# Optimization experiments

Measured on AMD Instinct MI355X. Metric: run time of the kernel, lower is better.

Reference implementation:

```python
import jax, jax.numpy as jnp
import numpy as np

N = 100000        # num nodes
E2 = 3200000      # num directed edges (symmetric)
D = 256           # node feature dim
C = 40            # num classes
NIDS = 1000       # labelled node ids
TOL = 0.01
MAXITER = 16
AVG_DEG = E2 // N // 2 * 2  # ~32


def setup_inputs() -> dict:
    key = jax.random.key(0)
    k1, k2, k3, k4, k5, k6 = jax.random.split(key, 6)
    E = E2 // 2
    row_h = jax.random.randint(k1, (E,), 0, N, dtype=jnp.int32)
    col_h = jax.random.randint(k2, (E,), 0, N, dtype=jnp.int32)
    # symmetrize so I - (1-eps)*A is SPD-like (CG assumption)
    row = jnp.concatenate([row_h, col_h])
    col = jnp.concatenate([col_h, row_h])
    vals = jax.random.uniform(k3, (E,), dtype=jnp.float32) * (0.9 / 32.0)
    data = jnp.concatenate([vals, vals])
    node_features = jax.random.normal(k4, (N, D), dtype=jnp.float32)
    ids = jax.random.randint(k5, (NIDS,), 0, N, dtype=jnp.int32)
    # hk.Linear with TruncatedNormal(stddev=1/sqrt(D)) init
    W = (jax.random.truncated_normal(k6, -2.0, 2.0, (D, C), dtype=jnp.float32)
         * (1.0 / np.sqrt(D))).astype(jnp.float32)
    b = jnp.zeros((C,), jnp.float32)
    e0 = jnp.zeros((), jnp.float32)  # hk.get_parameter('e0', (), init=zeros)
    return dict(node_features=node_features, W=W, b=b, e0=e0,
                data=data, row=row, col=col, ids=ids)


def reference(node_features, W, b, e0, data, row, col, ids):
    epsilon = jax.nn.sigmoid(e0)
    # head_transform=None; d_feat > num_classes -> Linear first, then smooth
    x = node_features @ W + b  # [N, C]

    def spmv(v):  # adj @ v for COO adjacency, v: [N, C]
        return jax.ops.segment_sum(data[:, None] * v[col], row, num_segments=N)

    def f(v):  # (I - (1-eps) A) v
        return v - (1.0 - epsilon) * spmv(v)

    # smooth(): x.shape[1] (=C) <= ids.size -> direct CG on dense x, then gather ids
    sol, _ = jax.scipy.sparse.linalg.cg(f, x, tol=TOL, maxiter=MAXITER)
    return sol[ids]  # [NIDS, C] logits
```

## Files before the change

### kernel.cpp

```cpp
#include <hip/hip_runtime.h>
#include <hip/hip_fp16.h>
#include <math.h>

#define NNODE  100000
#define NEDGE  3200000
#define DFEAT  256
#define NCLS   40
#define NC_TOT 4000000
#define NIDS   1000
#define TOLSQ  1.0e-4f
#define MAXIT  16

#define SB 2048
#define SLOT_TOT 1000000
#define SPB 489
#define XB 1024
#define VT 256
#define GR     128
#define GKC    32
#define GEMM_B 782

#define RB      128
#define NBUCK   782
#define BCAP    6144
#define SUBB    1024
#define NPB     800
#define EPB     4000

__device__ __forceinline__ float block_reduce_256(float v, float* red) {
  int tid = threadIdx.x;
  red[tid] = v;
  __syncthreads();
  #pragma unroll
  for (int off = 128; off > 0; off >>= 1) {
    if (tid < off) red[tid] += red[tid + off];
    __syncthreads();
  }
  float res = red[0];
  __syncthreads();
  return res;
}

__global__ void __launch_bounds__(256) k_pcount(const int* __restrict__ row,
                                                int* __restrict__ cntmat,
                                                int* __restrict__ total) {
  __shared__ int h[NBUCK];
  int tid = threadIdx.x, blk = blockIdx.x;
  for (int i = tid; i < NBUCK; i += 256) h[i] = 0;
  __syncthreads();
  int e0 = blk * EPB;
  for (int i = tid; i < EPB; i += 256) atomicAdd(&h[row[e0 + i] >> 7], 1);
  __syncthreads();
  for (int i = tid; i < NBUCK; i += 256) {
    int v = h[i];
    cntmat[blk * NBUCK + i] = v;
    if (v) atomicAdd(&total[i], v);
  }
}

__global__ void k_bscan2(const int* __restrict__ total, int* __restrict__ bptr) {
  __shared__ int s[1024];
  int tid = threadIdx.x;
  int v = (tid < NBUCK) ? total[tid] : 0;
  s[tid] = v;
  __syncthreads();
  for (int off = 1; off < 1024; off <<= 1) {
    int t = (tid >= off) ? s[tid - off] : 0;
    __syncthreads();
    s[tid] += t;
    __syncthreads();
  }
  if (tid < NBUCK) bptr[tid] = s[tid] - v;
  if (tid == 0) bptr[NBUCK] = NEDGE;
}

__global__ void __launch_bounds__(1024) k_colscan(int* __restrict__ cntmat,
                                                  const int* __restrict__ bptr) {
  __shared__ int s[1024];
  int b = blockIdx.x;
  int tid = threadIdx.x;
  int v = (tid < NPB) ? cntmat[tid * NBUCK + b] : 0;
  s[tid] = v;
  __syncthreads();
  for (int off = 1; off < 1024; off <<= 1) {
    int t = (tid >= off) ? s[tid - off] : 0;
    __syncthreads();
    s[tid] += t;
    __syncthreads();
  }
  if (tid < NPB) cntmat[tid * NBUCK + b] = bptr[b] + s[tid] - v;
}

__global__ void __launch_bounds__(256) k_ppart(const int* __restrict__ row,
    const int* __restrict__ col, const float* __restrict__ data,
    const int* __restrict__ offmat, uint2* __restrict__ bstage) {
  __shared__ int cnt[NBUCK];
  __shared__ int segs[NBUCK + 1];
  __shared__ int cur[NBUCK];
  __shared__ int goff[NBUCK];
  __shared__ int scp[256];
  __shared__ unsigned short bof[EPB];
  __shared__ uint2 pay[EPB];
  int tid = threadIdx.x, blk = blockIdx.x;
  int e0 = blk * EPB;

  for (int i = tid; i < NBUCK; i += 256) {
    cnt[i] = 0;
    goff[i] = offmat[blk * NBUCK + i];
  }
  __syncthreads();
  for (int i = tid; i < EPB; i += 256) atomicAdd(&cnt[row[e0 + i] >> 7], 1);
  __syncthreads();

  int t4 = tid * 4;
  int l0 = (t4 + 0 < NBUCK) ? cnt[t4 + 0] : 0;
  int l1 = (t4 + 1 < NBUCK) ? cnt[t4 + 1] : 0;
  int l2 = (t4 + 2 < NBUCK) ? cnt[t4 + 2] : 0;
  int l3 = (t4 + 3 < NBUCK) ? cnt[t4 + 3] : 0;
  int mysum = l0 + l1 + l2 + l3;
  scp[tid] = mysum;
  __syncthreads();
  for (int off = 1; off < 256; off <<= 1) {
    int t = (tid >= off) ? scp[tid - off] : 0;
    __syncthreads();
    scp[tid] += t;
    __syncthreads();
  }
  int base = scp[tid] - mysum;
  if (t4 + 0 <= NBUCK) segs[t4 + 0] = base;  base += l0;
  if (t4 + 1 <= NBUCK) segs[t4 + 1] = base;  base += l1;
  if (t4 + 2 <= NBUCK) segs[t4 + 2] = base;  base += l2;
  if (t4 + 3 <= NBUCK) segs[t4 + 3] = base;
  for (int i = tid; i < NBUCK; i += 256) cur[i] = 0;
  __syncthreads();

  for (int b = tid; b < NBUCK; b += 256) {
    int s1 = segs[b + 1];
    for (int i = segs[b]; i < s1; ++i) bof[i] = (unsigned short)b;
  }
  for (int i = tid; i < EPB; i += 256) {
    int rr = row[e0 + i];
    int b = rr >> 7;
    int rk = atomicAdd(&cur[b], 1);
    pay[segs[b] + rk] = make_uint2(((unsigned)(rr & (RB - 1)) << 17) | (unsigned)col[e0 + i],
                                   __float_as_uint(data[e0 + i]));
  }
  __syncthreads();
  for (int i = tid; i < EPB; i += 256) {
    int b = bof[i];
    bstage[goff[b] + (i - segs[b])] = pay[i];
  }
}

__global__ void __launch_bounds__(256) k_bbuild(const int* __restrict__ bptr,
    const uint2* __restrict__ bstage, int* __restrict__ rowptr,
    int2* __restrict__ csr) {
  __shared__ uint2 ebuf[BCAP];
  __shared__ int deg[SUBB];
  __shared__ int segs[SUBB];
  __shared__ int scp[256];
  int b = blockIdx.x;
  int s0 = bptr[b], s1 = bptr[b + 1];
  int n = s1 - s0;
  if (n > BCAP) n = BCAP;
  int tid = threadIdx.x;
  for (int i = tid; i < SUBB; i += 256) deg[i] = 0;
  __syncthreads();
  for (int i = tid; i < n; i += 256) {
    uint2 e = bstage[s0 + i];
    ebuf[i] = e;
    int key = (int)(e.x >> 17) * 8 + (int)((e.x & 0x1FFFF) >> 14);
    atomicAdd(&deg[key], 1);
  }
  __syncthreads();
  int t4 = tid * 4;
  int l0 = deg[t4 + 0], l1 = deg[t4 + 1], l2 = deg[t4 + 2], l3 = deg[t4 + 3];
  int mysum = l0 + l1 + l2 + l3;
  scp[tid] = mysum;
  __syncthreads();
  for (int off = 1; off < 256; off <<= 1) {
    int t = (tid >= off) ? scp[tid - off] : 0;
    __syncthreads();
    scp[tid] += t;
    __syncthreads();
  }
  int base = scp[tid] - mysum;
  segs[t4 + 0] = base;  base += l0;
  segs[t4 + 1] = base;  base += l1;
  segs[t4 + 2] = base;  base += l2;
  segs[t4 + 3] = base;
  __syncthreads();
  for (int i = tid; i < SUBB; i += 256) deg[i] = 0;
  if (tid < RB) {
    int grow = b * RB + tid;
    if (grow < NNODE) rowptr[grow] = s0 + segs[tid * 8];
  }
  if (b == 0 && tid == 0) rowptr[NNODE] = NEDGE;
  __syncthreads();
  for (int i = tid; i < n; i += 256) {
    uint2 e = ebuf[i];
    int col = (int)(e.x & 0x1FFFF);
    int key = (int)(e.x >> 17) * 8 + (col >> 14);
    int pos = atomicAdd(&deg[key], 1);
    csr[s0 + segs[key] + pos] = make_int2(col, (int)e.y);
  }
}

__global__ void __launch_bounds__(256) k_gemm(const float* __restrict__ feat,
    const float* __restrict__ W, const float* __restrict__ bias,
    float* __restrict__ r, float* __restrict__ p, __half* __restrict__ ph,
    float* __restrict__ part) {
  __shared__ float ftile[2][GR][GKC + 1];
  __shared__ float wtile[2][GKC * NCLS];
  __shared__ float red[256];
  int tid = threadIdx.x;
  int r0 = blockIdx.x * GR;
  int rl0 = (tid >> 2) * 2;
  int cbase = (tid & 3) * 10;
  float acc0[10], acc1[10];
  #pragma unroll
  for (int j = 0; j < 10; ++j) {
    float bv = bias[cbase + j];
    acc0[j] = bv;
    acc1[j] = bv;
  }

  float4 sf[4];
  float sw[5];
  int srr[4], skq[4];
  #pragma unroll
  for (int it = 0; it < 4; ++it) {
    int i = tid + it * 256;
    srr[it] = i >> 3;
    skq[it] = i & 7;
  }

  #pragma unroll
  for (int it = 0; it < 4; ++it) {
    int grow = r0 + srr[it];
    sf[it] = make_float4(0.f, 0.f, 0.f, 0.f);
    if (grow < NNODE)
      sf[it] = *(const float4*)(feat + (size_t)grow * DFEAT + skq[it] * 4);
  }
  #pragma unroll
  for (int it = 0; it < 5; ++it) sw[it] = W[tid + it * 256];
  #pragma unroll
  for (int it = 0; it < 4; ++it) {
    ftile[0][srr[it]][skq[it] * 4 + 0] = sf[it].x;
    ftile[0][srr[it]][skq[it] * 4 + 1] = sf[it].y;
    ftile[0][srr[it]][skq[it] * 4 + 2] = sf[it].z;
    ftile[0][srr[it]][skq[it] * 4 + 3] = sf[it].w;
  }
  #pragma unroll
  for (int it = 0; it < 5; ++it) wtile[0][tid + it * 256] = sw[it];
  __syncthreads();

  for (int t = 0; t < DFEAT / GKC; ++t) {
    if (t + 1 < DFEAT / GKC) {
      int k0n = (t + 1) * GKC;
      #pragma unroll
      for (int it = 0; it < 4; ++it) {
        int grow = r0 + srr[it];
        sf[it] = make_float4(0.f, 0.f, 0.f, 0.f);
        if (grow < NNODE)
          sf[it] = *(const float4*)(feat + (size_t)grow * DFEAT + k0n + skq[it] * 4);
      }
      #pragma unroll
      for (int it = 0; it < 5; ++it) sw[it] = W[k0n * NCLS + tid + it * 256];
    }
    int buf = t & 1;
    #pragma unroll 4
    for (int kk = 0; kk < GKC; ++kk) {
      float f0 = ftile[buf][rl0][kk];
      float f1 = ftile[buf][rl0 + 1][kk];
      const float* wr = &wtile[buf][kk * NCLS + cbase];
      #pragma unroll
      for (int j = 0; j < 10; ++j) {
        float w = wr[j];
        acc0[j] = fmaf(f0, w, acc0[j]);
        acc1[j] = fmaf(f1, w, acc1[j]);
      }
    }
    if (t + 1 < DFEAT / GKC) {
      int nb = (t + 1) & 1;
      #pragma unroll
      for (int it = 0; it < 4; ++it) {
        ftile[nb][srr[it]][skq[it] * 4 + 0] = sf[it].x;
        ftile[nb][srr[it]][skq[it] * 4 + 1] = sf[it].y;
        ftile[nb][srr[it]][skq[it] * 4 + 2] = sf[it].z;
        ftile[nb][srr[it]][skq[it] * 4 + 3] = sf[it].w;
      }
      #pragma unroll
      for (int it = 0; it < 5; ++it) wtile[nb][tid + it * 256] = sw[it];
      __syncthreads();
    }
  }

  float local = 0.f;
  int g0 = r0 + rl0, g1 = g0 + 1;
  if (g0 < NNODE) {
    size_t b0 = (size_t)g0 * NCLS + cbase;
    #pragma unroll
    for (int j = 0; j < 10; ++j) {
      float a = acc0[j];
      r[b0 + j] = a; p[b0 + j] = a; ph[b0 + j] = __float2half(a);
      local = fmaf(a, a, local);
    }
  }
  if (g1 < NNODE) {
    size_t b1 = (size_t)g1 * NCLS + cbase;
    #pragma unroll
    for (int j = 0; j < 10; ++j) {
      float a = acc1[j];
      r[b1 + j] = a; p[b1 + j] = a; ph[b1 + j] = __float2half(a);
      local = fmaf(a, a, local);
    }
  }
  float tot = block_reduce_256(local, red);
  if (tid == 0) part[blockIdx.x] = tot;
}

__global__ void k_init_scal(const float* __restrict__ part, const float* __restrict__ e0,
                            float* __restrict__ scal) {
  __shared__ float red[256];
  float local = 0.f;
  for (int i = threadIdx.x; i < GEMM_B; i += 256) local += part[i];
  float bs = block_reduce_256(local, red);
  if (threadIdx.x == 0) {
    float eps = 1.f / (1.f + expf(-e0[0]));
    scal[0] = 1.f - eps;
    scal[1] = TOLSQ * bs;
    scal[2] = bs;
  }
}

__global__ void __launch_bounds__(VT) k_spmv(const float* __restrict__ scal, int k,
    const int* __restrict__ rowptr, const int2* __restrict__ csr,
    const __half* __restrict__ ph, const float* __restrict__ p,
    float* __restrict__ Ap, float* __restrict__ part) {
  float gamma = scal[2 + k], atol2 = scal[1];
  if (!(gamma > atol2)) return;
  float omega = scal[0];
  int b = blockIdx.x;
  int chunk = (b & 7) * (SB / 8) + (b >> 3);
  int sbase = chunk * SPB;
  float local = 0.f;
  #pragma unroll
  for (int it = 0; it < 2; ++it) {
    int li = threadIdx.x + it * VT;
    int s = sbase + li;
    if (li < SPB && s < SLOT_TOT) {
      int rr = s / 10;
      int cq4 = (s - rr * 10) * 4;
      int s0 = rowptr[rr], s1 = rowptr[rr + 1];
      float a0 = 0.f, a1 = 0.f, a2 = 0.f, a3 = 0.f;
      #pragma unroll 4
      for (int j = s0; j < s1; ++j) {
        int2 pr = csr[j];
        float w = __int_as_float(pr.y);
        uint2 g = *(const uint2*)(ph + (size_t)pr.x * NCLS + cq4);
        __half2 h01 = *(__half2*)&g.x;
        __half2 h23 = *(__half2*)&g.y;
        float2 f01 = __half22float2(h01);
        float2 f23 = __half22float2(h23);
        a0 = fmaf(w, f01.x, a0);
        a1 = fmaf(w, f01.y, a1);
        a2 = fmaf(w, f23.x, a2);
        a3 = fmaf(w, f23.y, a3);
      }
      size_t e = (size_t)rr * NCLS + cq4;
      float4 pe = *(const float4*)(p + e);
      float4 v;
      v.x = fmaf(-omega, a0, pe.x);
      v.y = fmaf(-omega, a1, pe.y);
      v.z = fmaf(-omega, a2, pe.z);
      v.w = fmaf(-omega, a3, pe.w);
      *(float4*)(Ap + e) = v;
      local = fmaf(pe.x, v.x, local);
      local = fmaf(pe.y, v.y, local);
      local = fmaf(pe.z, v.z, local);
      local = fmaf(pe.w, v.w, local);
    }
  }
  __shared__ float red[256];
  float tot = block_reduce_256(local, red);
  if (threadIdx.x == 0) part[blockIdx.x] = tot;
}

__global__ void __launch_bounds__(VT) k_xr(const float* __restrict__ scal, int k,
    const float* __restrict__ part_in,
    const float* __restrict__ p, const float* __restrict__ Ap,
    float* __restrict__ r, const int* __restrict__ ids,
    float* __restrict__ out, float* __restrict__ part_out) {
  float gamma = scal[2 + k], atol2 = scal[1];
  if (!(gamma > atol2)) return;
  __shared__ float red[256];
  float lp = 0.f;
  for (int i = threadIdx.x; i < SB; i += VT) lp += part_in[i];
  float pap = block_reduce_256(lp, red);
  float alpha = gamma / pap;
  int idx = blockIdx.x * VT + threadIdx.x;
  if (idx < NIDS * NCLS) {
    int i = idx / NCLS, c = idx - (idx / NCLS) * NCLS;
    out[idx] += alpha * p[(size_t)ids[i] * NCLS + c];
  }
  const float4* a4 = (const float4*)Ap;
  float4* r4 = (float4*)r;
  float local = 0.f;
  int stride = gridDim.x * blockDim.x;
  for (int e = blockIdx.x * blockDim.x + threadIdx.x; e < NC_TOT / 4; e += stride) {
    float4 ae = a4[e], re = r4[e];
    re.x = fmaf(-alpha, ae.x, re.x); re.y = fmaf(-alpha, ae.y, re.y);
    re.z = fmaf(-alpha, ae.z, re.z); re.w = fmaf(-alpha, ae.w, re.w);
    r4[e] = re;
    local = fmaf(re.x, re.x, local); local = fmaf(re.y, re.y, local);
    local = fmaf(re.z, re.z, local); local = fmaf(re.w, re.w, local);
  }
  float tot = block_reduce_256(local, red);
  if (threadIdx.x == 0) part_out[blockIdx.x] = tot;
}

__global__ void __launch_bounds__(VT) k_pupd(float* __restrict__ scal, int k,
    const float* __restrict__ part_in,
    const float* __restrict__ r, float* __restrict__ p, __half* __restrict__ ph) {
  float gamma = scal[2 + k], atol2 = scal[1];
  if (!(gamma > atol2)) {
    if (blockIdx.x == 0 && threadIdx.x == 0) scal[2 + k + 1] = gamma;
    return;
  }
  __shared__ float red[256];
  float lp = 0.f;
  for (int i = threadIdx.x; i < XB; i += VT) lp += part_in[i];
  float gnew = block_reduce_256(lp, red);
  float beta = gnew / gamma;
  const float4* r4 = (const float4*)r;
  float4* p4 = (float4*)p;
  int stride = gridDim.x * blockDim.x;
  for (int e = blockIdx.x * blockDim.x + threadIdx.x; e < NC_TOT / 4; e += stride) {
    float4 pe = p4[e], re = r4[e];
    pe.x = fmaf(beta, pe.x, re.x); pe.y = fmaf(beta, pe.y, re.y);
    pe.z = fmaf(beta, pe.z, re.z); pe.w = fmaf(beta, pe.w, re.w);
    p4[e] = pe;
    int e4 = e * 4;
    ph[e4 + 0] = __float2half(pe.x);
    ph[e4 + 1] = __float2half(pe.y);
    ph[e4 + 2] = __float2half(pe.z);
    ph[e4 + 3] = __float2half(pe.w);
  }
  if (blockIdx.x == 0 && threadIdx.x == 0) scal[2 + k + 1] = gnew;
}

extern "C" void kernel_launch(void* const* d_in, const int* in_sizes, int n_in,
                              void* d_out, int out_size, void* d_ws, size_t ws_size,
                              hipStream_t stream) {
  const float* feat = (const float*)d_in[0];
  const float* W    = (const float*)d_in[1];
  const float* bias = (const float*)d_in[2];
  const float* e0   = (const float*)d_in[3];
  const float* data = (const float*)d_in[4];
  const int*   row  = (const int*)d_in[5];
  const int*   col  = (const int*)d_in[6];
  const int*   ids  = (const int*)d_in[7];
  float* out = (float*)d_out;

  size_t off = 0;
  char* base = (char*)d_ws;
  auto take = [&](size_t nbytes) -> void* {
    void* ptr = base + off;
    off += (nbytes + 255) & ~(size_t)255;
    return ptr;
  };
  float* rv  = (float*)take((size_t)NC_TOT * 4);
  float* pv  = (float*)take((size_t)NC_TOT * 4);
  float* ap  = (float*)take((size_t)NC_TOT * 4);
  __half* ph = (__half*)take((size_t)NC_TOT * 2);
  int2*  csr = (int2*)take((size_t)NEDGE * 8);
  int* rowptr    = (int*)take((size_t)(NNODE + 1) * 4);
  int* cntmat    = (int*)take((size_t)NPB * NBUCK * 4);
  int* total     = (int*)take((size_t)(NBUCK + 2) * 4);
  int* bptr      = (int*)take((size_t)(NBUCK + 2) * 4);
  float* part_a  = (float*)take(SB * 4);
  float* part_b  = (float*)take(XB * 4);
  float* scal    = (float*)take(64 * 4);

  uint2* bstage = (uint2*)rv;

  hipMemsetAsync(total, 0, (size_t)(NBUCK + 2) * 4, stream);
  hipMemsetAsync(out, 0, (size_t)NIDS * NCLS * 4, stream);
  k_pcount<<<NPB, 256, 0, stream>>>(row, cntmat, total);
  k_bscan2<<<1, 1024, 0, stream>>>(total, bptr);
  k_colscan<<<NBUCK, 1024, 0, stream>>>(cntmat, bptr);
  k_ppart<<<NPB, 256, 0, stream>>>(row, col, data, cntmat, bstage);
  k_bbuild<<<NBUCK, 256, 0, stream>>>(bptr, bstage, rowptr, csr);

  k_gemm<<<GEMM_B, 256, 0, stream>>>(feat, W, bias, rv, pv, ph, part_a);
  k_init_scal<<<1, 256, 0, stream>>>(part_a, e0, scal);

  for (int k = 0; k < MAXIT; ++k) {
    k_spmv<<<SB, VT, 0, stream>>>(scal, k, rowptr, csr, ph, pv, ap, part_a);
    k_xr  <<<XB, VT, 0, stream>>>(scal, k, part_a, pv, ap, rv, ids, out, part_b);
    k_pupd<<<XB, VT, 0, stream>>>(scal, k, part_b, rv, pv, ph);
  }
}
```

Before: 421.7 us.

## Split half-precision search vector into two 20-class column groups for SpMV gathers

Stores the fp16 copy of p as two separate planes of 20 classes per node instead of one 40-class row. The SpMV handles one plane at a time per block, so the gather footprint per pass is half the size and can stay in cache better. The GEMM and p-update kernels write the new layout, and the p-update now packs its fp16 stores into a single 8-byte write. The cost is that the CSR index and weight stream is read twice per SpMV, once per plane.

```diff
diff --git a/kernel.cpp b/kernel.cpp
--- a/kernel.cpp
+++ b/kernel.cpp
@@ -11,9 +11,10 @@
 #define TOLSQ  1.0e-4f
 #define MAXIT  16
 
-#define SB 2048
-#define SLOT_TOT 1000000
-#define SPB 489
+#define SB 1536
+#define SLOT_G 500000
+#define SPB2 326
+#define GRP_H 2000000
 #define XB 1024
 #define VT 256
 #define GR     128
@@ -217,6 +218,8 @@
   int r0 = blockIdx.x * GR;
   int rl0 = (tid >> 2) * 2;
   int cbase = (tid & 3) * 10;
+  int gg = (cbase >= 20) ? 1 : 0;
+  int cqb = cbase - gg * 20;
   float acc0[10], acc1[10];
   #pragma unroll
   for (int j = 0; j < 10; ++j) {
@@ -300,19 +303,21 @@
   int g0 = r0 + rl0, g1 = g0 + 1;
   if (g0 < NNODE) {
     size_t b0 = (size_t)g0 * NCLS + cbase;
+    size_t h0 = (size_t)gg * GRP_H + (size_t)g0 * 20 + cqb;
     #pragma unroll
     for (int j = 0; j < 10; ++j) {
       float a = acc0[j];
-      r[b0 + j] = a; p[b0 + j] = a; ph[b0 + j] = __float2half(a);
+      r[b0 + j] = a; p[b0 + j] = a; ph[h0 + j] = __float2half(a);
       local = fmaf(a, a, local);
     }
   }
   if (g1 < NNODE) {
     size_t b1 = (size_t)g1 * NCLS + cbase;
+    size_t h1 = (size_t)gg * GRP_H + (size_t)g1 * 20 + cqb;
     #pragma unroll
     for (int j = 0; j < 10; ++j) {
       float a = acc1[j];
-      r[b1 + j] = a; p[b1 + j] = a; ph[b1 + j] = __float2half(a);
+      r[b1 + j] = a; p[b1 + j] = a; ph[h1 + j] = __float2half(a);
       local = fmaf(a, a, local);
     }
   }
@@ -343,43 +348,47 @@
   float omega = scal[0];
   int b = blockIdx.x;
   int chunk = (b & 7) * (SB / 8) + (b >> 3);
-  int sbase = chunk * SPB;
+  int sbase = chunk * SPB2;
   float local = 0.f;
   #pragma unroll
-  for (int it = 0; it < 2; ++it) {
-    int li = threadIdx.x + it * VT;
-    int s = sbase + li;
-    if (li < SPB && s < SLOT_TOT) {
-      int rr = s / 10;
-      int cq4 = (s - rr * 10) * 4;
-      int s0 = rowptr[rr], s1 = rowptr[rr + 1];
-      float a0 = 0.f, a1 = 0.f, a2 = 0.f, a3 = 0.f;
-      #pragma unroll 4
-      for (int j = s0; j < s1; ++j) {
-        int2 pr = csr[j];
-        float w = __int_as_float(pr.y);
-        uint2 g = *(const uint2*)(ph + (size_t)pr.x * NCLS + cq4);
-        __half2 h01 = *(__half2*)&g.x;
-        __half2 h23 = *(__half2*)&g.y;
-        float2 f01 = __half22float2(h01);
-        float2 f23 = __half22float2(h23);
-        a0 = fmaf(w, f01.x, a0);
-        a1 = fmaf(w, f01.y, a1);
-        a2 = fmaf(w, f23.x, a2);
-        a3 = fmaf(w, f23.y, a3);
+  for (int g = 0; g < 2; ++g) {
+    const __half* __restrict__ phg = ph + (size_t)g * GRP_H;
+    #pragma unroll
+    for (int it = 0; it < 2; ++it) {
+      int li = threadIdx.x + it * VT;
+      int s = sbase + li;
+      if (li < SPB2 && s < SLOT_G) {
+        int rr = s / 5;
+        int q = s - rr * 5;
+        int s0 = rowptr[rr], s1 = rowptr[rr + 1];
+        float a0 = 0.f, a1 = 0.f, a2 = 0.f, a3 = 0.f;
+        #pragma unroll 4
+        for (int j = s0; j < s1; ++j) {
+          int2 pr = csr[j];
+          float w = __int_as_float(pr.y);
+          uint2 gv = *(const uint2*)(phg + (size_t)pr.x * 20 + q * 4);
+          __half2 h01 = *(__half2*)&gv.x;
+          __half2 h23 = *(__half2*)&gv.y;
+          float2 f01 = __half22float2(h01);
+          float2 f23 = __half22float2(h23);
+          a0 = fmaf(w, f01.x, a0);
+          a1 = fmaf(w, f01.y, a1);
+          a2 = fmaf(w, f23.x, a2);
+          a3 = fmaf(w, f23.y, a3);
+        }
+        size_t e = (size_t)rr * NCLS + g * 20 + q * 4;
+        float4 pe = *(const float4*)(p + e);
+        float4 v;
+        v.x = fmaf(-omega, a0, pe.x);
+        v.y = fmaf(-omega, a1, pe.y);
+        v.z = fmaf(-omega, a2, pe.z);
+        v.w = fmaf(-omega, a3, pe.w);
+        *(float4*)(Ap + e) = v;
+        local = fmaf(pe.x, v.x, local);
+        local = fmaf(pe.y, v.y, local);
+        local = fmaf(pe.z, v.z, local);
+        local = fmaf(pe.w, v.w, local);
       }
-      size_t e = (size_t)rr * NCLS + cq4;
-      float4 pe = *(const float4*)(p + e);
-      float4 v;
-      v.x = fmaf(-omega, a0, pe.x);
-      v.y = fmaf(-omega, a1, pe.y);
-      v.z = fmaf(-omega, a2, pe.z);
-      v.w = fmaf(-omega, a3, pe.w);
-      *(float4*)(Ap + e) = v;
-      local = fmaf(pe.x, v.x, local);
-      local = fmaf(pe.y, v.y, local);
-      local = fmaf(pe.z, v.z, local);
-      local = fmaf(pe.w, v.w, local);
     }
   }
   __shared__ float red[256];
@@ -441,11 +450,16 @@
     pe.x = fmaf(beta, pe.x, re.x); pe.y = fmaf(beta, pe.y, re.y);
     pe.z = fmaf(beta, pe.z, re.z); pe.w = fmaf(beta, pe.w, re.w);
     p4[e] = pe;
-    int e4 = e * 4;
-    ph[e4 + 0] = __float2half(pe.x);
-    ph[e4 + 1] = __float2half(pe.y);
-    ph[e4 + 2] = __float2half(pe.z);
-    ph[e4 + 3] = __float2half(pe.w);
+    int rr = e / 10;
+    int c = (e - rr * 10) * 4;
+    int g = (c >= 20) ? 1 : 0;
+    int cq = c - g * 20;
+    __half2 h01 = __floats2half2_rn(pe.x, pe.y);
+    __half2 h23 = __floats2half2_rn(pe.z, pe.w);
+    uint2 pack;
+    pack.x = *(unsigned*)&h01;
+    pack.y = *(unsigned*)&h23;
+    *(uint2*)(ph + (size_t)g * GRP_H + (size_t)rr * 20 + cq) = pack;
   }
   if (blockIdx.x == 0 && threadIdx.x == 0) scal[2 + k + 1] = gnew;
 }
```

After: 483.5 us. +14.7%, slower.
